# Kernel tuning notes

Hardware: AMD Instinct MI355X
Metric: run time of the kernel (lower is better)

The kernel has to match this reference:

```python
import jax, jax.numpy as jnp
import numpy as np

B, NUM_OBJECTS, NUM_ATTRS, T = 8, 128, 4, 12
MAX_CONCEPTS, EMBED_DIM, IDENTITY_DIM, ATTENTION_DIM, HIDDEN_DIM = 2048, 128, 64, 64, 256
OP_MODE, OP_INSERT, OP_TRANSFER = 0, 1, 2


def setup_inputs() -> dict:
    key = jax.random.key(0)
    ks = jax.random.split(key, 24)
    def rn(k, shape, s=0.05):
        return s * jax.random.normal(k, shape, dtype=jnp.float32)
    return {
        'scene': jax.random.randint(ks[0], (B, NUM_OBJECTS, NUM_ATTRS), 0, MAX_CONCEPTS - 1),
        'program_op': jax.random.randint(ks[1], (B, T), 0, 3),
        'program_arg': jax.random.randint(ks[2], (B, T), 0, MAX_CONCEPTS),
        'attr_emb_in': rn(ks[3], (MAX_CONCEPTS, EMBED_DIM)),
        'attr_emb_out': rn(ks[4], (MAX_CONCEPTS, EMBED_DIM)),
        'attr_emb_id': rn(ks[5], (MAX_CONCEPTS, IDENTITY_DIM)),
        'concept_emb_in': rn(ks[6], (MAX_CONCEPTS, EMBED_DIM)),
        'concept_emb_out': rn(ks[7], (MAX_CONCEPTS, EMBED_DIM)),
        'concept_emb_id': rn(ks[8], (MAX_CONCEPTS, IDENTITY_DIM)),
        'embed_init': rn(ks[9], (EMBED_DIM,)),
        'identity_init': rn(ks[10], (IDENTITY_DIM,)),
        'attention_init': jnp.zeros((ATTENTION_DIM,), dtype=jnp.float32),
        'axon_w1': rn(ks[11], (HIDDEN_DIM, ATTENTION_DIM + IDENTITY_DIM)),
        'axon_b1': rn(ks[12], (HIDDEN_DIM,)),
        'axon_w2': rn(ks[13], (ATTENTION_DIM, HIDDEN_DIM)),
        'axon_b2': rn(ks[14], (ATTENTION_DIM,)),
        'meta_w1': rn(ks[15], (HIDDEN_DIM, EMBED_DIM + ATTENTION_DIM)),
        'meta_b1': rn(ks[16], (HIDDEN_DIM,)),
        'meta_w2': rn(ks[17], (ATTENTION_DIM, HIDDEN_DIM)),
        'meta_b2': rn(ks[18], (ATTENTION_DIM,)),
    }


def _mlp(x, w1, b1, w2, b2):
    # torch Linear convention: y = x @ W.T + b
    return jnp.maximum(x @ w1.T + b1, 0.0) @ w2.T + b2


def reference(scene, program_op, program_arg, attr_emb_in, attr_emb_out, attr_emb_id,
              concept_emb_in, concept_emb_out, concept_emb_id,
              embed_init, identity_init, attention_init,
              axon_w1, axon_b1, axon_w2, axon_b2,
              meta_w1, meta_b1, meta_w2, meta_b2):
    Bq, N, _ = scene.shape
    C = MAX_CONCEPTS + N  # dim_concept
    mask = (scene != -1).astype(jnp.float32)  # (B,N,A) non-background mask
    def embed_bg(E):
        return (E[scene + 1] * mask[..., None]).sum(2)  # (B,N,D)
    objects_in = embed_bg(attr_emb_in)
    objects_out = embed_bg(attr_emb_out)
    objects_id = embed_bg(attr_emb_id)

    rep = lambda w: jnp.broadcast_to(w[None], (Bq,) + w.shape)
    dendron = jnp.concatenate([rep(concept_emb_in), objects_in], 1)    # (B,C,E)
    axon = jnp.concatenate([rep(concept_emb_out), objects_out], 1)     # (B,C,E)
    identity = jnp.concatenate([rep(concept_emb_id), objects_id], 1)   # (B,C,Id)
    weight_matrix = jnp.einsum('bie,bje->bij', dendron, axon)           # (B,C,C)

    arguments = concept_emb_out[program_arg]                            # (B,T,E)
    is_mode = (program_op == OP_MODE).astype(jnp.float32)               # (B,T)
    is_insert = (program_op == OP_INSERT).astype(jnp.float32)
    is_transfer = (program_op == OP_TRANSFER).astype(jnp.float32)

    meta0 = jnp.broadcast_to(attention_init[None], (Bq, ATTENTION_DIM))
    att0 = jnp.broadcast_to(attention_init[None, None], (Bq, C, ATTENTION_DIM))

    def step(carry, xs):
        meta, attention = carry
        arg_i, m, ins, tr = xs  # (B,E), (B,), (B,), (B,)
        new_meta = _mlp(jnp.concatenate([meta, arg_i], 1), meta_w1, meta_b1, meta_w2, meta_b2)
        meta = m[:, None] * new_meta + (1.0 - m[:, None]) * meta
        # (arguments * axon).mean over embed dim -> (B,C)
        proj = jnp.einsum('be,bce->bc', arg_i, axon) / EMBED_DIM
        attention_insert = meta[:, None, :] * proj[:, :, None]          # (B,C,A)
        attended_weight = weight_matrix * attention.mean(2)[:, None, :] # (B,C,C)
        ia = jnp.concatenate([identity, attention], 2)                  # (B,C,Id+A)
        # (attended_weight[:,:,:,None] * ia[:,None]).mean(2) == matmul / C
        gathered = jnp.einsum('bij,bjd->bid', attended_weight, ia) / C  # (B,C,Id+A)
        attention_transfer = _mlp(gathered, axon_w1, axon_b1, axon_w2, axon_b2) + gathered[..., IDENTITY_DIM:]
        attention = attention + ins[:, None, None] * attention_insert + tr[:, None, None] * attention_transfer
        attention = jnp.clip(jnp.where(attention >= 0, attention, 0.01 * attention), -1.0, 2.0)
        return (meta, attention), (attention, attention_insert, attention_transfer)

    xs = (jnp.swapaxes(arguments, 0, 1), is_mode.T, is_insert.T, is_transfer.T)
    (meta, attention), (att_hist, ins_hist, trans_hist) = jax.lax.scan(step, (meta0, att0), xs)
    output_softmax = jax.nn.log_softmax(attention.mean(2), axis=1)  # (B,C)
    return (output_softmax, att_hist, ins_hist, trans_hist)
```

## Files before the change

### kernel.cpp

```cpp
#include <hip/hip_runtime.h>

#define B 8
#define NOBJ 128
#define NATTR 4
#define T 12
#define MC 2048
#define E 128
#define IDD 64
#define AD 64
#define HD 256
#define C 2176

typedef short s16x8 __attribute__((ext_vector_type(8)));
typedef float f32x4 __attribute__((ext_vector_type(4)));

__device__ inline unsigned short f2b(float f) {
  union { float f; unsigned u; } v; v.f = f;
  unsigned r = v.u + 0x7FFFu + ((v.u >> 16) & 1u);
  return (unsigned short)(r >> 16);
}
__device__ inline float b2f(unsigned short u) {
  union { unsigned u; float f; } v; v.u = ((unsigned)u) << 16;
  return v.f;
}

__device__ __forceinline__ void st_coh_u64(unsigned long long* p, unsigned long long v) {
  __hip_atomic_store(p, v, __ATOMIC_RELAXED, __HIP_MEMORY_SCOPE_AGENT);
}
__device__ __forceinline__ unsigned long long ld_coh_u64(const unsigned long long* p) {
  return __hip_atomic_load(p, __ATOMIC_RELAXED, __HIP_MEMORY_SCOPE_AGENT);
}
__device__ __forceinline__ void st_coh_u32(unsigned* p, unsigned v) {
  __hip_atomic_store(p, v, __ATOMIC_RELAXED, __HIP_MEMORY_SCOPE_AGENT);
}
__device__ __forceinline__ unsigned ld_coh_u32(const unsigned* p) {
  return __hip_atomic_load(p, __ATOMIC_RELAXED, __HIP_MEMORY_SCOPE_AGENT);
}

__device__ __forceinline__ int gidx(int r, int c) {
  return r * 128 + ((((c >> 3) ^ (r & 15)) << 3) | (c & 7));
}
__device__ __forceinline__ int hidx(int r, int c) {
  return r * 256 + ((((c >> 3) ^ (r & 15)) << 3) | (c & 7));
}
__device__ __forceinline__ int mtidx(int r, int c) {
  return r * 128 + ((((c >> 3) ^ (r & 15)) << 3) | (c & 7));
}

__global__ __launch_bounds__(256) void k_setup1(
    const int* __restrict__ scene,
    const float* __restrict__ aein, const float* __restrict__ aeout,
    const float* __restrict__ aeid,
    const float* __restrict__ cein, const float* __restrict__ ceout,
    const float* __restrict__ ceid,
    const float* __restrict__ aw1, const float* __restrict__ aw2,
    const float* __restrict__ mw1, const float* __restrict__ mw2,
    unsigned short* __restrict__ dendron_bf, float* __restrict__ axon,
    float* __restrict__ identity,
    unsigned short* __restrict__ w1_bf, unsigned short* __restrict__ w2_bf,
    float* __restrict__ mw1T, float* __restrict__ mw2T,
    unsigned* __restrict__ mflag) {
  int blk = blockIdx.x;
  int tid = threadIdx.x;
  if (blk < 4352) {
    int gid = blk * 2 + (tid >> 7);
    int e = tid & 127;
    int b = gid / C, j = gid % C;
    float din, dout, did = 0.f;
    if (j < MC) {
      din  = cein[j * E + e];
      dout = ceout[j * E + e];
      if (e < IDD) did = ceid[j * IDD + e];
    } else {
      int obj = j - MC;
      float sIn = 0.f, sOut = 0.f, sId = 0.f;
      for (int a = 0; a < NATTR; a++) {
        int s = scene[(b * NOBJ + obj) * NATTR + a];
        float m = (s != -1) ? 1.f : 0.f;
        int idx = s + 1;
        sIn  += aein[idx * E + e] * m;
        sOut += aeout[idx * E + e] * m;
        if (e < IDD) sId += aeid[idx * IDD + e] * m;
      }
      din = sIn; dout = sOut; did = sId;
    }
    dendron_bf[(size_t)gid * E + e] = f2b(din);
    axon[(size_t)gid * E + e] = dout;
    if (e < IDD) identity[(size_t)gid * IDD + e] = did;
  } else if (blk < 4544) {
    int i = (blk - 4352) * 256 + tid;
    if (i < HD * E)  w1_bf[i] = f2b(aw1[i]);
    if (i < AD * HD) w2_bf[i] = f2b(aw2[i]);
    if (i < 192 * HD) { int c = i / HD, k = i % HD; mw1T[c * HD + k] = mw1[k * 192 + c]; }
    if (i < HD * AD)  { int k = i / AD, a = i % AD; mw2T[k * AD + a] = mw2[a * HD + k]; }
  } else {
    if (tid < B * 16) mflag[tid] = 0u;
  }
}

__global__ __launch_bounds__(256) void k_setup2(
    const float* __restrict__ axon, const float* __restrict__ identity,
    const float* __restrict__ att_init,
    const int* __restrict__ prog_op, const int* __restrict__ prog_arg,
    const float* __restrict__ ceout,
    const float* __restrict__ mw1T, const float* __restrict__ mb1,
    const float* __restrict__ mw2T, const float* __restrict__ mb2,
    unsigned short* __restrict__ axonT, unsigned short* __restrict__ idT_g,
    unsigned short* __restrict__ siaT, float* __restrict__ att_g,
    float* __restrict__ meta_all, float* __restrict__ proj_all) {
  int blk = blockIdx.x;
  int tid = threadIdx.x;
  if (blk < 272) {
    int b = blk / 34, jc = blk % 34;
    int j0 = jc * 64;
    __shared__ float ax[64][129];
    __shared__ float idb[64][65];
    int lane = tid & 63, lr = lane & 15;
    float s = att_init[lane];
    s += __shfl_xor(s, 1, 64);  s += __shfl_xor(s, 2, 64);
    s += __shfl_xor(s, 4, 64);  s += __shfl_xor(s, 8, 64);
    s += __shfl_xor(s, 16, 64); s += __shfl_xor(s, 32, 64);
    float am0 = s * (1.f / AD);
    for (int i = tid; i < 64 * 128; i += 256) {
      int j = i >> 7, e = i & 127;
      ax[j][e] = axon[(size_t)(b * C + j0 + j) * E + e];
    }
    for (int i = tid; i < 64 * 64; i += 256) {
      int j = i >> 6, d = i & 63;
      idb[j][d] = identity[(size_t)(b * C + j0 + j) * IDD + d];
    }
    __syncthreads();
    for (int i = tid; i < 128 * 64; i += 256) {
      int e = i >> 6, jj = i & 63;
      axonT[(size_t)(b * E + e) * C + j0 + jj] = f2b(ax[jj][e]);
    }
    for (int i = tid; i < 64 * 64; i += 256) {
      int d = i >> 6, jj = i & 63;
      idT_g[(size_t)(b * 64 + d) * C + j0 + jj] = f2b(idb[jj][d]);
      siaT[(size_t)(b * 128 + d) * C + j0 + jj] = f2b(idb[jj][d] * am0);
      siaT[(size_t)(b * 128 + 64 + d) * C + j0 + jj] = f2b(att_init[d] * am0);
    }
    {
      float* ag = att_g + (size_t)blk * 4096 + tid * 16;
      #pragma unroll
      for (int n = 0; n < 4; n++) {
        float v0 = att_init[n * 16 + lr];
        #pragma unroll
        for (int v = 0; v < 4; v++) ag[n * 4 + v] = v0;
      }
    }
  } else if (blk < 280) {
    int b = blk - 272;
    __shared__ float x[192];
    __shared__ float h[HD];
    __shared__ float meta[AD];
    if (tid < AD) meta[tid] = att_init[tid];
    __syncthreads();
    for (int t = 0; t < T; t++) {
      int arg = prog_arg[b * T + t];
      if (tid < AD) x[tid] = meta[tid];
      else if (tid < 192) x[tid] = ceout[arg * E + (tid - 64)];
      __syncthreads();
      float s = mb1[tid];
      for (int c = 0; c < 192; c++) s += x[c] * mw1T[c * HD + tid];
      h[tid] = fmaxf(s, 0.f);
      __syncthreads();
      if (tid < AD) {
        float o = mb2[tid];
        for (int k = 0; k < HD; k++) o += h[k] * mw2T[k * AD + tid];
        float m = (prog_op[b * T + t] == 0) ? 1.f : 0.f;
        float nm = m * o + (1.f - m) * meta[tid];
        meta[tid] = nm;
        meta_all[(t * B + b) * AD + tid] = nm;
      }
      __syncthreads();
    }
  } else {
    int gid = (blk - 280) * 4 + (tid >> 6);
    int lane = tid & 63;
    int b = gid / C, i = gid % C;
    float a0 = axon[(size_t)gid * E + lane];
    float a1 = axon[(size_t)gid * E + 64 + lane];
    for (int t = 0; t < T; t++) {
      int arg = prog_arg[b * T + t];
      float p = a0 * ceout[arg * E + lane] + a1 * ceout[arg * E + 64 + lane];
      for (int off = 1; off < 64; off <<= 1) p += __shfl_xor(p, off, 64);
      if (lane == 0) proj_all[(size_t)(t * B + b) * C + i] = p * (1.f / E);
    }
  }
}

__global__ __launch_bounds__(256) void k_step(
    int t,
    const unsigned short* __restrict__ dendron_bf,
    const unsigned short* __restrict__ axonT,
    const unsigned short* __restrict__ idT_g,
    const unsigned short* __restrict__ siaT_in,
    const unsigned short* __restrict__ w1_bf, const float* __restrict__ b1g,
    const unsigned short* __restrict__ w2_bf, const float* __restrict__ b2g,
    const float* __restrict__ proj_all, const float* __restrict__ meta_all,
    const int* __restrict__ prog_op,
    unsigned long long* __restrict__ Mt64,
    float* __restrict__ att_g, unsigned short* __restrict__ siaT_out,
    float* __restrict__ rowmean,
    float* __restrict__ att_hist, float* __restrict__ ins_hist,
    float* __restrict__ trans_hist,
    unsigned* __restrict__ mflag) {
  const int blk = blockIdx.x;
  const int b = blk / 34, ch = blk % 34, j0 = ch * 64;
  const int tid = threadIdx.x;
  const int w = tid >> 6, lane = tid & 63, lr = lane & 15, lg = lane >> 4;

  __shared__ unsigned short smem[24576];
  __shared__ float am_l[64];
  unsigned short* g_l = smem;
  unsigned short* mt  = smem + 8192;
  unsigned short* h_l = smem + 8192;
  float* mred = (float*)smem;

  const f32x4 z = {0.f, 0.f, 0.f, 0.f};
  const unsigned ph = (unsigned)(t + 1);

  float att[4][4];
  {
    const f32x4* ag = (const f32x4*)(att_g + (size_t)blk * 4096 + tid * 16);
    #pragma unroll
    for (int n = 0; n < 4; n++) {
      f32x4 v4 = ag[n];
      #pragma unroll
      for (int v = 0; v < 4; v++) att[n][v] = v4[v];
    }
  }

  if (ch < 16) {
    int d0 = (ch >> 2) * 32, e0 = (ch & 3) * 32;
    const unsigned short* ap0 = siaT_in + (size_t)(b * 128 + d0 + lr) * C + w * 544 + lg * 8;
    const unsigned short* ap1 = ap0 + (size_t)16 * C;
    const unsigned short* bp0 = axonT + (size_t)(b * E + e0 + lr) * C + w * 544 + lg * 8;
    const unsigned short* bp1 = bp0 + (size_t)16 * C;
    f32x4 a00 = z, a01 = z, a10 = z, a11 = z;
    #pragma unroll 4
    for (int kk = 0; kk < 17; kk++) {
      int k0 = kk * 32;
      s16x8 A0 = *(const s16x8*)(ap0 + k0);
      s16x8 A1 = *(const s16x8*)(ap1 + k0);
      s16x8 B0 = *(const s16x8*)(bp0 + k0);
      s16x8 B1 = *(const s16x8*)(bp1 + k0);
      a00 = __builtin_amdgcn_mfma_f32_16x16x32_bf16(A0, B0, a00, 0, 0, 0);
      a01 = __builtin_amdgcn_mfma_f32_16x16x32_bf16(A0, B1, a01, 0, 0, 0);
      a10 = __builtin_amdgcn_mfma_f32_16x16x32_bf16(A1, B0, a10, 0, 0, 0);
      a11 = __builtin_amdgcn_mfma_f32_16x16x32_bf16(A1, B1, a11, 0, 0, 0);
    }
    #pragma unroll
    for (int v = 0; v < 4; v++) {
      mred[(w * 32 + lg * 4 + v) * 33 + lr]          = a00[v];
      mred[(w * 32 + lg * 4 + v) * 33 + 16 + lr]     = a01[v];
      mred[(w * 32 + 16 + lg * 4 + v) * 33 + lr]     = a10[v];
      mred[(w * 32 + 16 + lg * 4 + v) * 33 + 16 + lr] = a11[v];
    }
    __syncthreads();
    {
      int r = tid >> 3, c = (tid & 7) * 4;
      float s0 = 0.f, s1 = 0.f, s2 = 0.f, s3 = 0.f;
      #pragma unroll
      for (int w4 = 0; w4 < 4; w4++) {
        const float* p = &mred[(w4 * 32 + r) * 33 + c];
        s0 += p[0]; s1 += p[1]; s2 += p[2]; s3 += p[3];
      }
      unsigned long long pk = (unsigned long long)f2b(s0)
                            | ((unsigned long long)f2b(s1) << 16)
                            | ((unsigned long long)f2b(s2) << 32)
                            | ((unsigned long long)f2b(s3) << 48);
      st_coh_u64(Mt64 + (((size_t)(b * 128 + d0 + r) * 128) + e0 + c) / 4, pk);
    }
    asm volatile("s_waitcnt vmcnt(0)" ::: "memory");
    __syncthreads();
    if (tid == 0) st_coh_u32(mflag + b * 16 + ch, ph);
  }
  if (tid < 16) {
    while (ld_coh_u32(mflag + b * 16 + tid) < ph) __builtin_amdgcn_s_sleep(1);
  }
  __syncthreads();
  {
    const unsigned long long* mtp = Mt64 + (size_t)b * 4096;
    #pragma unroll
    for (int k = 0; k < 16; k++) {
      int idx = tid + k * 256;
      unsigned long long v = ld_coh_u64(mtp + idx);
      int r = idx >> 5, c4 = (idx & 31) * 4;
      *(unsigned long long*)&mt[mtidx(r, c4)] = v;
    }
  }
  __syncthreads();
  {
    s16x8 afr[4];
    #pragma unroll
    for (int ke = 0; ke < 4; ke++)
      afr[ke] = *(const s16x8*)(dendron_bf + (size_t)(b * C + j0 + w * 16 + lr) * E + ke * 32 + lg * 8);
    #pragma unroll
    for (int n = 0; n < 8; n++) {
      f32x4 acc = z;
      #pragma unroll
      for (int ke = 0; ke < 4; ke++) {
        s16x8 bf = *(const s16x8*)&mt[mtidx(n * 16 + lr, ke * 32 + lg * 8)];
        acc = __builtin_amdgcn_mfma_f32_16x16x32_bf16(afr[ke], bf, acc, 0, 0, 0);
      }
      #pragma unroll
      for (int v = 0; v < 4; v++)
        g_l[gidx(w * 16 + lg * 4 + v, n * 16 + lr)] = f2b(acc[v] * (1.f / C));
    }
  }
  __syncthreads();
  {
    s16x8 gf[4];
    #pragma unroll
    for (int kd = 0; kd < 4; kd++)
      gf[kd] = *(const s16x8*)&g_l[gidx(w * 16 + lr, kd * 32 + lg * 8)];
    #pragma unroll
    for (int n = 0; n < 16; n++) {
      f32x4 acc = z;
      #pragma unroll
      for (int kd = 0; kd < 4; kd++) {
        s16x8 bf = *(const s16x8*)(w1_bf + (size_t)(n * 16 + lr) * E + kd * 32 + lg * 8);
        acc = __builtin_amdgcn_mfma_f32_16x16x32_bf16(gf[kd], bf, acc, 0, 0, 0);
      }
      float b1v = b1g[n * 16 + lr];
      #pragma unroll
      for (int v = 0; v < 4; v++)
        h_l[hidx(w * 16 + lg * 4 + v, n * 16 + lr)] = f2b(fmaxf(acc[v] + b1v, 0.f));
    }
  }
  __syncthreads();
  {
    s16x8 hf[8];
    #pragma unroll
    for (int kk = 0; kk < 8; kk++)
      hf[kk] = *(const s16x8*)&h_l[hidx(w * 16 + lr, kk * 32 + lg * 8)];
    int op = prog_op[b * T + t];
    float insF = (op == 1) ? 1.f : 0.f, trF = (op == 2) ? 1.f : 0.f;
    float projv[4];
    #pragma unroll
    for (int v = 0; v < 4; v++)
      projv[v] = proj_all[(size_t)(t * B + b) * C + j0 + w * 16 + lg * 4 + v];
    #pragma unroll
    for (int n = 0; n < 4; n++) {
      f32x4 acc = z;
      #pragma unroll
      for (int kk = 0; kk < 8; kk++) {
        s16x8 bf = *(const s16x8*)(w2_bf + (size_t)(n * 16 + lr) * HD + kk * 32 + lg * 8);
        acc = __builtin_amdgcn_mfma_f32_16x16x32_bf16(hf[kk], bf, acc, 0, 0, 0);
      }
      int a = n * 16 + lr;
      float b2v = b2g[a];
      float meta_a = meta_all[(size_t)(t * B + b) * AD + a];
      #pragma unroll
      for (int v = 0; v < 4; v++) {
        int row = lg * 4 + v;
        int i = j0 + w * 16 + row;
        float transfer = acc[v] + b2v + b2f(g_l[gidx(w * 16 + row, 64 + a)]);
        float insert = meta_a * projv[v];
        float attv = att[n][v] + insF * insert + trF * transfer;
        attv = (attv >= 0.f) ? attv : 0.01f * attv;
        attv = fminf(fmaxf(attv, -1.f), 2.f);
        att[n][v] = attv;
        size_t hi = (((size_t)t * B + b) * C + i) * AD + a;
        __builtin_nontemporal_store(attv, att_hist + hi);
        __builtin_nontemporal_store(insert, ins_hist + hi);
        __builtin_nontemporal_store(transfer, trans_hist + hi);
      }
    }
  }
  float amr[4];
  {
    float s[4];
    #pragma unroll
    for (int v = 0; v < 4; v++) s[v] = att[0][v] + att[1][v] + att[2][v] + att[3][v];
    #pragma unroll
    for (int v = 0; v < 4; v++) {
      s[v] += __shfl_xor(s[v], 1, 64);
      s[v] += __shfl_xor(s[v], 2, 64);
      s[v] += __shfl_xor(s[v], 4, 64);
      s[v] += __shfl_xor(s[v], 8, 64);
      amr[v] = s[v] * (1.f / AD);
    }
    if (lr == 0) {
      #pragma unroll
      for (int v = 0; v < 4; v++) {
        am_l[w * 16 + lg * 4 + v] = amr[v];
        rowmean[(size_t)b * C + j0 + w * 16 + lg * 4 + v] = amr[v];
      }
    }
  }
  {
    f32x4* ag = (f32x4*)(att_g + (size_t)blk * 4096 + tid * 16);
    #pragma unroll
    for (int n = 0; n < 4; n++) {
      f32x4 v4;
      #pragma unroll
      for (int v = 0; v < 4; v++) v4[v] = att[n][v];
      ag[n] = v4;
      unsigned long long pk = 0;
      #pragma unroll
      for (int v = 0; v < 4; v++)
        pk |= (unsigned long long)f2b(att[n][v] * amr[v]) << (16 * v);
      *(unsigned long long*)(siaT_out + (size_t)(b * 128 + 64 + n * 16 + lr) * C + j0 + w * 16 + lg * 4) = pk;
    }
  }
  __syncthreads();
  #pragma unroll
  for (int k = 0; k < 2; k++) {
    int idx = tid + k * 256;
    int d = idx >> 3, part = idx & 7;
    int j = part * 8;
    s16x8 iv = *(const s16x8*)(idT_g + (size_t)(b * 64 + d) * C + j0 + j);
    s16x8 ov;
    #pragma unroll
    for (int m = 0; m < 8; m++)
      ov[m] = (short)f2b(b2f((unsigned short)iv[m]) * am_l[j + m]);
    *(s16x8*)(siaT_out + (size_t)(b * 128 + d) * C + j0 + j) = ov;
  }
}

__global__ void k_softmax(const float* __restrict__ rowmean, float* __restrict__ out) {
  int b = blockIdx.x;
  __shared__ float am[C];
  __shared__ float red[256];
  int tid = threadIdx.x;
  for (int i = tid; i < C; i += 256) am[i] = rowmean[(size_t)b * C + i];
  __syncthreads();
  float mx = -1e30f;
  for (int i = tid; i < C; i += 256) mx = fmaxf(mx, am[i]);
  red[tid] = mx; __syncthreads();
  for (int s = 128; s > 0; s >>= 1) { if (tid < s) red[tid] = fmaxf(red[tid], red[tid + s]); __syncthreads(); }
  mx = red[0]; __syncthreads();
  float sm = 0.f;
  for (int i = tid; i < C; i += 256) sm += expf(am[i] - mx);
  red[tid] = sm; __syncthreads();
  for (int s = 128; s > 0; s >>= 1) { if (tid < s) red[tid] += red[tid + s]; __syncthreads(); }
  float lse = logf(red[0]) + mx;
  for (int i = tid; i < C; i += 256) out[(size_t)b * C + i] = am[i] - lse;
}

extern "C" void kernel_launch(void* const* d_in, const int* in_sizes, int n_in,
                              void* d_out, int out_size, void* d_ws, size_t ws_size,
                              hipStream_t stream) {
  const int* scene     = (const int*)d_in[0];
  const int* prog_op   = (const int*)d_in[1];
  const int* prog_arg  = (const int*)d_in[2];
  const float* aein    = (const float*)d_in[3];
  const float* aeout   = (const float*)d_in[4];
  const float* aeid    = (const float*)d_in[5];
  const float* cein    = (const float*)d_in[6];
  const float* ceout   = (const float*)d_in[7];
  const float* ceid    = (const float*)d_in[8];
  const float* att_init = (const float*)d_in[11];
  const float* aw1 = (const float*)d_in[12];
  const float* ab1 = (const float*)d_in[13];
  const float* aw2 = (const float*)d_in[14];
  const float* ab2 = (const float*)d_in[15];
  const float* mw1 = (const float*)d_in[16];
  const float* mb1 = (const float*)d_in[17];
  const float* mw2 = (const float*)d_in[18];
  const float* mb2 = (const float*)d_in[19];

  char* ws = (char*)d_ws;
  size_t off = 0;
  auto carve = [&](size_t bytes) { char* p = ws + off; off += (bytes + 255) & ~(size_t)255; return p; };
  float* axon      = (float*)carve((size_t)B * C * E * 4);
  float* identity  = (float*)carve((size_t)B * C * IDD * 4);
  float* proj_all  = (float*)carve((size_t)T * B * C * 4);
  float* meta_all  = (float*)carve((size_t)T * B * AD * 4);
  float* mw1T      = (float*)carve((size_t)192 * HD * 4);
  float* mw2T      = (float*)carve((size_t)HD * AD * 4);
  float* rowmean   = (float*)carve((size_t)B * C * 4);
  float* att_g     = (float*)carve((size_t)272 * 4096 * 4);
  unsigned short* dendron_bf = (unsigned short*)carve((size_t)B * C * E * 2);
  unsigned short* axonT      = (unsigned short*)carve((size_t)B * E * C * 2);
  unsigned short* idT_g      = (unsigned short*)carve((size_t)B * 64 * C * 2);
  unsigned short* siaT       = (unsigned short*)carve((size_t)B * 128 * C * 2);
  unsigned long long* Mt64   = (unsigned long long*)carve((size_t)B * 4096 * 8);
  unsigned short* w1_bf      = (unsigned short*)carve((size_t)HD * E * 2);
  unsigned short* w2_bf      = (unsigned short*)carve((size_t)AD * HD * 2);
  unsigned*       mflag      = (unsigned*)carve(1024);

  float* out_sm     = (float*)d_out;
  float* att_hist   = out_sm + B * C;
  float* ins_hist   = att_hist + (size_t)T * B * C * AD;
  float* trans_hist = ins_hist + (size_t)T * B * C * AD;

  k_setup1<<<dim3(4545), dim3(256), 0, stream>>>(scene, aein, aeout, aeid, cein, ceout, ceid,
                                                 aw1, aw2, mw1, mw2,
                                                 dendron_bf, axon, identity,
                                                 w1_bf, w2_bf, mw1T, mw2T, mflag);
  k_setup2<<<dim3(1368), dim3(256), 0, stream>>>(axon, identity, att_init,
                                                 prog_op, prog_arg, ceout,
                                                 mw1T, mb1, mw2T, mb2,
                                                 axonT, idT_g, siaT, att_g,
                                                 meta_all, proj_all);
  for (int t = 0; t < T; t++) {
    k_step<<<dim3(272), dim3(256), 0, stream>>>(t, dendron_bf, axonT, idT_g, siaT,
                                                w1_bf, ab1, w2_bf, ab2,
                                                proj_all, meta_all, prog_op,
                                                Mt64, att_g, siaT, rowmean,
                                                att_hist, ins_hist, trans_hist, mflag);
  }
  k_softmax<<<dim3(B), dim3(256), 0, stream>>>(rowmean, out_sm);
}
```

Before: 655.4 us.

## Replace cross-block flag sync with redundant per-block Mt GEMM and double-buffered sia

Before, 16 of the 34 chunk blocks per batch each computed a slice of the 128x128 reduction matrix, published it to global memory, and every block spin-waited on flags before reading it. Now every block computes the full 128x128 matrix itself, staging 128-wide K slices through swizzled LDS, so the flags, the spin-wait and the coherent stores go away. The sia buffer is ping-ponged between two arrays so that reads of the previous step never race with writes of the next. The cost is roughly 34x redundant GEMM work over the full C dimension per batch, a larger LDS footprint, and rowmean is now written only on the last step.

```diff
diff --git a/kernel.cpp b/kernel.cpp
--- a/kernel.cpp
+++ b/kernel.cpp
@@ -22,19 +22,6 @@
 __device__ inline float b2f(unsigned short u) {
   union { unsigned u; float f; } v; v.u = ((unsigned)u) << 16;
   return v.f;
-}
-
-__device__ __forceinline__ void st_coh_u64(unsigned long long* p, unsigned long long v) {
-  __hip_atomic_store(p, v, __ATOMIC_RELAXED, __HIP_MEMORY_SCOPE_AGENT);
-}
-__device__ __forceinline__ unsigned long long ld_coh_u64(const unsigned long long* p) {
-  return __hip_atomic_load(p, __ATOMIC_RELAXED, __HIP_MEMORY_SCOPE_AGENT);
-}
-__device__ __forceinline__ void st_coh_u32(unsigned* p, unsigned v) {
-  __hip_atomic_store(p, v, __ATOMIC_RELAXED, __HIP_MEMORY_SCOPE_AGENT);
-}
-__device__ __forceinline__ unsigned ld_coh_u32(const unsigned* p) {
-  return __hip_atomic_load(p, __ATOMIC_RELAXED, __HIP_MEMORY_SCOPE_AGENT);
 }
 
 __device__ __forceinline__ int gidx(int r, int c) {
@@ -58,8 +45,7 @@
     unsigned short* __restrict__ dendron_bf, float* __restrict__ axon,
     float* __restrict__ identity,
     unsigned short* __restrict__ w1_bf, unsigned short* __restrict__ w2_bf,
-    float* __restrict__ mw1T, float* __restrict__ mw2T,
-    unsigned* __restrict__ mflag) {
+    float* __restrict__ mw1T, float* __restrict__ mw2T) {
   int blk = blockIdx.x;
   int tid = threadIdx.x;
   if (blk < 4352) {
@@ -87,14 +73,12 @@
     dendron_bf[(size_t)gid * E + e] = f2b(din);
     axon[(size_t)gid * E + e] = dout;
     if (e < IDD) identity[(size_t)gid * IDD + e] = did;
-  } else if (blk < 4544) {
+  } else {
     int i = (blk - 4352) * 256 + tid;
     if (i < HD * E)  w1_bf[i] = f2b(aw1[i]);
     if (i < AD * HD) w2_bf[i] = f2b(aw2[i]);
     if (i < 192 * HD) { int c = i / HD, k = i % HD; mw1T[c * HD + k] = mw1[k * 192 + c]; }
     if (i < HD * AD)  { int k = i / AD, a = i % AD; mw2T[k * AD + a] = mw2[a * HD + k]; }
-  } else {
-    if (tid < B * 16) mflag[tid] = 0u;
   }
 }
 
@@ -190,36 +174,34 @@
   }
 }
 
-__global__ __launch_bounds__(256) void k_step(
+__global__ __launch_bounds__(256, 2) void k_step(
     int t,
     const unsigned short* __restrict__ dendron_bf,
     const unsigned short* __restrict__ axonT,
     const unsigned short* __restrict__ idT_g,
-    const unsigned short* __restrict__ siaT_in,
+    const unsigned short* __restrict__ siaA,
+    unsigned short* __restrict__ siaB,
     const unsigned short* __restrict__ w1_bf, const float* __restrict__ b1g,
     const unsigned short* __restrict__ w2_bf, const float* __restrict__ b2g,
     const float* __restrict__ proj_all, const float* __restrict__ meta_all,
     const int* __restrict__ prog_op,
-    unsigned long long* __restrict__ Mt64,
-    float* __restrict__ att_g, unsigned short* __restrict__ siaT_out,
-    float* __restrict__ rowmean,
+    float* __restrict__ att_g, float* __restrict__ rowmean,
     float* __restrict__ att_hist, float* __restrict__ ins_hist,
-    float* __restrict__ trans_hist,
-    unsigned* __restrict__ mflag) {
+    float* __restrict__ trans_hist) {
   const int blk = blockIdx.x;
   const int b = blk / 34, ch = blk % 34, j0 = ch * 64;
   const int tid = threadIdx.x;
   const int w = tid >> 6, lane = tid & 63, lr = lane & 15, lg = lane >> 4;
 
-  __shared__ unsigned short smem[24576];
+  __shared__ unsigned short smem[32768];
   __shared__ float am_l[64];
-  unsigned short* g_l = smem;
-  unsigned short* mt  = smem + 8192;
-  unsigned short* h_l = smem + 8192;
-  float* mred = (float*)smem;
+  unsigned short* stgA = smem;
+  unsigned short* stgB = smem + 16384;
+  unsigned short* mt   = smem;
+  unsigned short* h_l  = smem;
+  unsigned short* g_l  = smem + 16384;
 
   const f32x4 z = {0.f, 0.f, 0.f, 0.f};
-  const unsigned ph = (unsigned)(t + 1);
 
   float att[4][4];
   {
@@ -232,65 +214,55 @@
     }
   }
 
-  if (ch < 16) {
-    int d0 = (ch >> 2) * 32, e0 = (ch & 3) * 32;
-    const unsigned short* ap0 = siaT_in + (size_t)(b * 128 + d0 + lr) * C + w * 544 + lg * 8;
-    const unsigned short* ap1 = ap0 + (size_t)16 * C;
-    const unsigned short* bp0 = axonT + (size_t)(b * E + e0 + lr) * C + w * 544 + lg * 8;
-    const unsigned short* bp1 = bp0 + (size_t)16 * C;
-    f32x4 a00 = z, a01 = z, a10 = z, a11 = z;
-    #pragma unroll 4
-    for (int kk = 0; kk < 17; kk++) {
-      int k0 = kk * 32;
-      s16x8 A0 = *(const s16x8*)(ap0 + k0);
-      s16x8 A1 = *(const s16x8*)(ap1 + k0);
-      s16x8 B0 = *(const s16x8*)(bp0 + k0);
-      s16x8 B1 = *(const s16x8*)(bp1 + k0);
-      a00 = __builtin_amdgcn_mfma_f32_16x16x32_bf16(A0, B0, a00, 0, 0, 0);
-      a01 = __builtin_amdgcn_mfma_f32_16x16x32_bf16(A0, B1, a01, 0, 0, 0);
-      a10 = __builtin_amdgcn_mfma_f32_16x16x32_bf16(A1, B0, a10, 0, 0, 0);
-      a11 = __builtin_amdgcn_mfma_f32_16x16x32_bf16(A1, B1, a11, 0, 0, 0);
-    }
-    #pragma unroll
-    for (int v = 0; v < 4; v++) {
-      mred[(w * 32 + lg * 4 + v) * 33 + lr]          = a00[v];
-      mred[(w * 32 + lg * 4 + v) * 33 + 16 + lr]     = a01[v];
-      mred[(w * 32 + 16 + lg * 4 + v) * 33 + lr]     = a10[v];
-      mred[(w * 32 + 16 + lg * 4 + v) * 33 + 16 + lr] = a11[v];
-    }
+  f32x4 acc[4][4];
+  #pragma unroll
+  for (int dt = 0; dt < 4; dt++)
+    #pragma unroll
+    for (int n = 0; n < 4; n++) acc[dt][n] = z;
+  const int d0 = (w >> 1) * 64, e0 = (w & 1) * 64;
+  const unsigned short* gAb = siaA + (size_t)b * 128 * C;
+  const unsigned short* gBb = axonT + (size_t)b * E * C;
+  for (int kc = 0; kc < 17; kc++) {
     __syncthreads();
-    {
-      int r = tid >> 3, c = (tid & 7) * 4;
-      float s0 = 0.f, s1 = 0.f, s2 = 0.f, s3 = 0.f;
-      #pragma unroll
-      for (int w4 = 0; w4 < 4; w4++) {
-        const float* p = &mred[(w4 * 32 + r) * 33 + c];
-        s0 += p[0]; s1 += p[1]; s2 += p[2]; s3 += p[3];
-      }
-      unsigned long long pk = (unsigned long long)f2b(s0)
-                            | ((unsigned long long)f2b(s1) << 16)
-                            | ((unsigned long long)f2b(s2) << 32)
-                            | ((unsigned long long)f2b(s3) << 48);
-      st_coh_u64(Mt64 + (((size_t)(b * 128 + d0 + r) * 128) + e0 + c) / 4, pk);
-    }
-    asm volatile("s_waitcnt vmcnt(0)" ::: "memory");
+    const unsigned short* gA = gAb + kc * 128;
+    const unsigned short* gB = gBb + kc * 128;
+    #pragma unroll
+    for (int q = 0; q < 8; q++) {
+      int idx = tid + q * 256;
+      int row = idx >> 4, slot = idx & 15;
+      int ds = row * 128 + ((slot ^ (row & 15)) << 3);
+      *(s16x8*)&stgA[ds] = *(const s16x8*)(gA + (size_t)row * C + slot * 8);
+      *(s16x8*)&stgB[ds] = *(const s16x8*)(gB + (size_t)row * C + slot * 8);
+    }
     __syncthreads();
-    if (tid == 0) st_coh_u32(mflag + b * 16 + ch, ph);
-  }
-  if (tid < 16) {
-    while (ld_coh_u32(mflag + b * 16 + tid) < ph) __builtin_amdgcn_s_sleep(1);
-  }
-  __syncthreads();
-  {
-    const unsigned long long* mtp = Mt64 + (size_t)b * 4096;
-    #pragma unroll
-    for (int k = 0; k < 16; k++) {
-      int idx = tid + k * 256;
-      unsigned long long v = ld_coh_u64(mtp + idx);
-      int r = idx >> 5, c4 = (idx & 31) * 4;
-      *(unsigned long long*)&mt[mtidx(r, c4)] = v;
-    }
-  }
+    #pragma unroll
+    for (int ks = 0; ks < 4; ks++) {
+      s16x8 af[4], bfr[4];
+      #pragma unroll
+      for (int dt = 0; dt < 4; dt++) {
+        int r = d0 + dt * 16 + lr;
+        af[dt] = *(const s16x8*)&stgA[r * 128 + (((ks * 4 + lg) ^ (r & 15)) << 3)];
+      }
+      #pragma unroll
+      for (int n = 0; n < 4; n++) {
+        int r = e0 + n * 16 + lr;
+        bfr[n] = *(const s16x8*)&stgB[r * 128 + (((ks * 4 + lg) ^ (r & 15)) << 3)];
+      }
+      #pragma unroll
+      for (int n = 0; n < 4; n++)
+        #pragma unroll
+        for (int dt = 0; dt < 4; dt++)
+          acc[dt][n] = __builtin_amdgcn_mfma_f32_16x16x32_bf16(af[dt], bfr[n], acc[dt][n], 0, 0, 0);
+    }
+  }
+  __syncthreads();
+  #pragma unroll
+  for (int dt = 0; dt < 4; dt++)
+    #pragma unroll
+    for (int n = 0; n < 4; n++)
+      #pragma unroll
+      for (int v = 0; v < 4; v++)
+        mt[mtidx(d0 + dt * 16 + lg * 4 + v, e0 + n * 16 + lr)] = f2b(acc[dt][n][v]);
   __syncthreads();
   {
     s16x8 afr[4];
@@ -299,15 +271,15 @@
       afr[ke] = *(const s16x8*)(dendron_bf + (size_t)(b * C + j0 + w * 16 + lr) * E + ke * 32 + lg * 8);
     #pragma unroll
     for (int n = 0; n < 8; n++) {
-      f32x4 acc = z;
+      f32x4 a2 = z;
       #pragma unroll
       for (int ke = 0; ke < 4; ke++) {
         s16x8 bf = *(const s16x8*)&mt[mtidx(n * 16 + lr, ke * 32 + lg * 8)];
-        acc = __builtin_amdgcn_mfma_f32_16x16x32_bf16(afr[ke], bf, acc, 0, 0, 0);
+        a2 = __builtin_amdgcn_mfma_f32_16x16x32_bf16(afr[ke], bf, a2, 0, 0, 0);
       }
       #pragma unroll
       for (int v = 0; v < 4; v++)
-        g_l[gidx(w * 16 + lg * 4 + v, n * 16 + lr)] = f2b(acc[v] * (1.f / C));
+        g_l[gidx(w * 16 + lg * 4 + v, n * 16 + lr)] = f2b(a2[v] * (1.f / C));
     }
   }
   __syncthreads();
@@ -318,16 +290,16 @@
       gf[kd] = *(const s16x8*)&g_l[gidx(w * 16 + lr, kd * 32 + lg * 8)];
     #pragma unroll
     for (int n = 0; n < 16; n++) {
-      f32x4 acc = z;
+      f32x4 a2 = z;
       #pragma unroll
       for (int kd = 0; kd < 4; kd++) {
         s16x8 bf = *(const s16x8*)(w1_bf + (size_t)(n * 16 + lr) * E + kd * 32 + lg * 8);
-        acc = __builtin_amdgcn_mfma_f32_16x16x32_bf16(gf[kd], bf, acc, 0, 0, 0);
+        a2 = __builtin_amdgcn_mfma_f32_16x16x32_bf16(gf[kd], bf, a2, 0, 0, 0);
       }
       float b1v = b1g[n * 16 + lr];
       #pragma unroll
       for (int v = 0; v < 4; v++)
-        h_l[hidx(w * 16 + lg * 4 + v, n * 16 + lr)] = f2b(fmaxf(acc[v] + b1v, 0.f));
+        h_l[hidx(w * 16 + lg * 4 + v, n * 16 + lr)] = f2b(fmaxf(a2[v] + b1v, 0.f));
     }
   }
   __syncthreads();
@@ -344,11 +316,11 @@
       projv[v] = proj_all[(size_t)(t * B + b) * C + j0 + w * 16 + lg * 4 + v];
     #pragma unroll
     for (int n = 0; n < 4; n++) {
-      f32x4 acc = z;
+      f32x4 a2 = z;
       #pragma unroll
       for (int kk = 0; kk < 8; kk++) {
         s16x8 bf = *(const s16x8*)(w2_bf + (size_t)(n * 16 + lr) * HD + kk * 32 + lg * 8);
-        acc = __builtin_amdgcn_mfma_f32_16x16x32_bf16(hf[kk], bf, acc, 0, 0, 0);
+        a2 = __builtin_amdgcn_mfma_f32_16x16x32_bf16(hf[kk], bf, a2, 0, 0, 0);
       }
       int a = n * 16 + lr;
       float b2v = b2g[a];
@@ -357,7 +329,7 @@
       for (int v = 0; v < 4; v++) {
         int row = lg * 4 + v;
         int i = j0 + w * 16 + row;
-        float transfer = acc[v] + b2v + b2f(g_l[gidx(w * 16 + row, 64 + a)]);
+        float transfer = a2[v] + b2v + b2f(g_l[gidx(w * 16 + row, 64 + a)]);
         float insert = meta_a * projv[v];
         float attv = att[n][v] + insF * insert + trF * transfer;
         attv = (attv >= 0.f) ? attv : 0.01f * attv;
@@ -385,10 +357,7 @@
     }
     if (lr == 0) {
       #pragma unroll
-      for (int v = 0; v < 4; v++) {
-        am_l[w * 16 + lg * 4 + v] = amr[v];
-        rowmean[(size_t)b * C + j0 + w * 16 + lg * 4 + v] = amr[v];
-      }
+      for (int v = 0; v < 4; v++) am_l[w * 16 + lg * 4 + v] = amr[v];
     }
   }
   {
@@ -403,13 +372,18 @@
       #pragma unroll
       for (int v = 0; v < 4; v++)
         pk |= (unsigned long long)f2b(att[n][v] * amr[v]) << (16 * v);
-      *(unsigned long long*)(siaT_out + (size_t)(b * 128 + 64 + n * 16 + lr) * C + j0 + w * 16 + lg * 4) = pk;
-    }
+      *(unsigned long long*)(siaB + (size_t)(b * 128 + 64 + n * 16 + lr) * C + j0 + w * 16 + lg * 4) = pk;
+    }
+  }
+  if (t == T - 1 && lr == 0) {
+    #pragma unroll
+    for (int v = 0; v < 4; v++)
+      rowmean[(size_t)b * C + j0 + w * 16 + lg * 4 + v] = amr[v];
   }
   __syncthreads();
   #pragma unroll
-  for (int k = 0; k < 2; k++) {
-    int idx = tid + k * 256;
+  for (int k2 = 0; k2 < 2; k2++) {
+    int idx = tid + k2 * 256;
     int d = idx >> 3, part = idx & 7;
     int j = part * 8;
     s16x8 iv = *(const s16x8*)(idT_g + (size_t)(b * 64 + d) * C + j0 + j);
@@ -417,7 +391,7 @@
     #pragma unroll
     for (int m = 0; m < 8; m++)
       ov[m] = (short)f2b(b2f((unsigned short)iv[m]) * am_l[j + m]);
-    *(s16x8*)(siaT_out + (size_t)(b * 128 + d) * C + j0 + j) = ov;
+    *(s16x8*)(siaB + (size_t)(b * 128 + d) * C + j0 + j) = ov;
   }
 }
 
@@ -477,32 +451,33 @@
   unsigned short* dendron_bf = (unsigned short*)carve((size_t)B * C * E * 2);
   unsigned short* axonT      = (unsigned short*)carve((size_t)B * E * C * 2);
   unsigned short* idT_g      = (unsigned short*)carve((size_t)B * 64 * C * 2);
-  unsigned short* siaT       = (unsigned short*)carve((size_t)B * 128 * C * 2);
-  unsigned long long* Mt64   = (unsigned long long*)carve((size_t)B * 4096 * 8);
+  unsigned short* siaT0      = (unsigned short*)carve((size_t)B * 128 * C * 2);
+  unsigned short* siaT1      = (unsigned short*)carve((size_t)B * 128 * C * 2);
   unsigned short* w1_bf      = (unsigned short*)carve((size_t)HD * E * 2);
   unsigned short* w2_bf      = (unsigned short*)carve((size_t)AD * HD * 2);
-  unsigned*       mflag      = (unsigned*)carve(1024);
 
   float* out_sm     = (float*)d_out;
   float* att_hist   = out_sm + B * C;
   float* ins_hist   = att_hist + (size_t)T * B * C * AD;
   float* trans_hist = ins_hist + (size_t)T * B * C * AD;
 
-  k_setup1<<<dim3(4545), dim3(256), 0, stream>>>(scene, aein, aeout, aeid, cein, ceout, ceid,
+  k_setup1<<<dim3(4544), dim3(256), 0, stream>>>(scene, aein, aeout, aeid, cein, ceout, ceid,
                                                  aw1, aw2, mw1, mw2,
                                                  dendron_bf, axon, identity,
-                                                 w1_bf, w2_bf, mw1T, mw2T, mflag);
+                                                 w1_bf, w2_bf, mw1T, mw2T);
   k_setup2<<<dim3(1368), dim3(256), 0, stream>>>(axon, identity, att_init,
                                                  prog_op, prog_arg, ceout,
                                                  mw1T, mb1, mw2T, mb2,
-                                                 axonT, idT_g, siaT, att_g,
+                                                 axonT, idT_g, siaT0, att_g,
                                                  meta_all, proj_all);
   for (int t = 0; t < T; t++) {
-    k_step<<<dim3(272), dim3(256), 0, stream>>>(t, dendron_bf, axonT, idT_g, siaT,
+    unsigned short* sin  = (t & 1) ? siaT1 : siaT0;
+    unsigned short* sout = (t & 1) ? siaT0 : siaT1;
+    k_step<<<dim3(272), dim3(256), 0, stream>>>(t, dendron_bf, axonT, idT_g, sin, sout,
                                                 w1_bf, ab1, w2_bf, ab2,
                                                 proj_all, meta_all, prog_op,
-                                                Mt64, att_g, siaT, rowmean,
-                                                att_hist, ins_hist, trans_hist, mflag);
+                                                att_g, rowmean,
+                                                att_hist, ins_hist, trans_hist);
   }
   k_softmax<<<dim3(B), dim3(256), 0, stream>>>(rowmean, out_sm);
 }
```

New measurement: 828.1 us. 26.4% more time.
